# Kernel tuning notes

Measured on AMD Instinct MI355X. Metric: run time of the kernel, lower is better.

## Reference

```python
import jax, jax.numpy as jnp
import numpy as np

B, S, E = 2, 2048, 2048
H, KV, D = 16, 4, 128
G = H // KV  # query heads per kv head
THETA = 10000.0


def setup_inputs() -> dict:
    key = jax.random.key(0)
    ks = jax.random.split(key, 5)
    scale = 0.02
    return {
        "x": jax.random.normal(ks[0], (B, S, E), dtype=jnp.float32),
        "Wq": jax.random.normal(ks[1], (E, H * D), dtype=jnp.float32) * scale,
        "Wk": jax.random.normal(ks[2], (E, KV * D), dtype=jnp.float32) * scale,
        "Wv": jax.random.normal(ks[3], (E, KV * D), dtype=jnp.float32) * scale,
        "Wo": jax.random.normal(ks[4], (E, E), dtype=jnp.float32) * scale,
    }


def _rope_tables(seq_len, head_dim, theta):
    inv_freq = 1.0 / theta ** (jnp.arange(0, head_dim, 2, dtype=jnp.float32) / head_dim)
    t = jnp.arange(seq_len, dtype=jnp.float32)
    freqs = jnp.outer(t, inv_freq)  # [S, D/2]
    cos = jnp.concatenate([jnp.cos(freqs), jnp.cos(freqs)], axis=-1)  # [S, D]
    sin = jnp.concatenate([jnp.sin(freqs), jnp.sin(freqs)], axis=-1)
    return cos, sin


def _apply_rope(x, cos, sin):
    # x: [B, h, S, D]; cos/sin: [S, D] broadcast over batch/heads
    d2 = x.shape[-1] // 2
    x1, x2 = x[..., :d2], x[..., d2:]
    rotated = jnp.concatenate([-x2, x1], axis=-1)
    return x * cos + rotated * sin


def reference(x, Wq, Wk, Wv, Wo):
    b, s, _ = x.shape
    q = (x @ Wq).reshape(b, s, H, D).transpose(0, 2, 1, 3)   # [B,H,S,D]
    k = (x @ Wk).reshape(b, s, KV, D).transpose(0, 2, 1, 3)  # [B,KV,S,D]
    v = (x @ Wv).reshape(b, s, KV, D).transpose(0, 2, 1, 3)

    cos, sin = _rope_tables(s, D, THETA)
    q = _apply_rope(q, cos, sin)
    k = _apply_rope(k, cos, sin)

    # GQA: q head h attends to kv head h // G (repeat_interleave order)
    qg = q.reshape(b, KV, G, s, D)
    scores = jnp.einsum("bkgsd,bktd->bkgst", qg, k) / jnp.sqrt(jnp.asarray(D, x.dtype))
    causal = jnp.tril(jnp.ones((s, s), dtype=bool))
    scores = jnp.where(causal, scores, jnp.asarray(-jnp.inf, scores.dtype))
    attn = jax.nn.softmax(scores, axis=-1)
    out = jnp.einsum("bkgst,bktd->bkgsd", attn, v)  # [B,KV,G,S,D]
    out = out.reshape(b, H, s, D).transpose(0, 2, 1, 3).reshape(b, s, H * D)
    return out @ Wo
```

## Files before the change

kernel.cpp:

```cpp
#include <hip/hip_runtime.h>
#include <stdint.h>

#define B_ 2
#define S_ 2048
#define E_ 2048
#define H_ 16
#define KV_ 4
#define D_ 128
#define G_ (H_ / KV_)
#define M_ (B_ * S_)

typedef unsigned short u16;
typedef unsigned int u32;
typedef __bf16 bf16x8 __attribute__((ext_vector_type(8)));
typedef float f32x4 __attribute__((ext_vector_type(4)));

__device__ __forceinline__ u16 f2bf(float f) {
  __bf16 h = (__bf16)f;
  return *(u16*)&h;
}
__device__ __forceinline__ float bf2f(u16 x) {
  return __uint_as_float(((u32)x) << 16);
}
__device__ __forceinline__ void store_c(u16* p, float v) { *p = f2bf(v); }
__device__ __forceinline__ void store_c(float* p, float v) { *p = v; }

__device__ __forceinline__ void gload_lds16(const u16* g, u16* lds) {
  __builtin_amdgcn_global_load_lds((const __attribute__((address_space(1))) u32*)g,
                                   (__attribute__((address_space(3))) u32*)lds,
                                   16, 0, 0);
}

__global__ __launch_bounds__(256) void convert_fp32_bf16(const float4* __restrict__ x,
                                                         uint2* __restrict__ o, int n4) {
  int i = blockIdx.x * 256 + threadIdx.x;
  if (i >= n4) return;
  float4 v = x[i];
  uint2 r;
  r.x = (u32)f2bf(v.x) | ((u32)f2bf(v.y) << 16);
  r.y = (u32)f2bf(v.z) | ((u32)f2bf(v.w) << 16);
  o[i] = r;
}

__global__ __launch_bounds__(256) void transpose_conv_w(const float* __restrict__ W,
                                                        u16* __restrict__ Wt,
                                                        int Kdim, int Ndim) {
  __shared__ float tile[32][33];
  int n0 = blockIdx.x * 32, k0 = blockIdx.y * 32;
  int tx = threadIdx.x, ty = threadIdx.y;
#pragma unroll
  for (int i = 0; i < 4; i++) {
    int r = ty + i * 8;
    tile[r][tx] = W[(size_t)(k0 + r) * Ndim + n0 + tx];
  }
  __syncthreads();
#pragma unroll
  for (int i = 0; i < 4; i++) {
    int r = ty + i * 8;
    Wt[(size_t)(n0 + r) * Kdim + k0 + tx] = f2bf(tile[tx][r]);
  }
}

__global__ __launch_bounds__(256) void transpose_v(const u16* __restrict__ V,
                                                   u16* __restrict__ Vt) {
  __shared__ u16 tile[32][33];
  int bkv = blockIdx.z;
  int b = bkv / KV_, kv = bkv % KV_;
  int s0 = blockIdx.x * 32, d0 = blockIdx.y * 32;
  int tx = threadIdx.x, ty = threadIdx.y;
#pragma unroll
  for (int i = 0; i < 4; i++) {
    int r = ty + i * 8;
    tile[r][tx] = V[((size_t)((b * S_ + s0 + r) * KV_ + kv)) * D_ + d0 + tx];
  }
  __syncthreads();
#pragma unroll
  for (int i = 0; i < 4; i++) {
    int r = ty + i * 8;
    Vt[((size_t)(b * KV_ + kv) * D_ + d0 + r) * S_ + s0 + tx] = tile[tx][r];
  }
}

__global__ __launch_bounds__(256) void rope_k_repack(const u16* __restrict__ Kin,
                                                     u16* __restrict__ Kp, int total) {
  int idx = blockIdx.x * 256 + threadIdx.x;
  if (idx >= total) return;
  int d = idx & 63;
  int rem = idx >> 6;
  int kv = rem % KV_;
  int row = rem / KV_;
  int b = row >> 11;
  int spos = row & (S_ - 1);
  size_t src = ((size_t)row * KV_ + kv) * D_ + d;
  float x0 = bf2f(Kin[src]);
  float x1 = bf2f(Kin[src + 64]);
  float ang = (float)spos * expf(-0.14391156831212787f * (float)d);
  float sn, cs;
  sincosf(ang, &sn, &cs);
  size_t dst = ((size_t)((b * KV_ + kv) * S_ + spos)) * D_ + d;
  Kp[dst]      = f2bf(x0 * cs - x1 * sn);
  Kp[dst + 64] = f2bf(x1 * cs + x0 * sn);
}

__global__ __launch_bounds__(256) void rope_q_inplace(u16* __restrict__ Qb, int total) {
  int idx = blockIdx.x * 256 + threadIdx.x;
  if (idx >= total) return;
  int d = idx & 63;
  int rem = idx >> 6;
  int h = rem & (H_ - 1);
  int row = rem >> 4;
  int spos = row & (S_ - 1);
  size_t base = ((size_t)row * H_ + h) * D_ + d;
  float x0 = bf2f(Qb[base]);
  float x1 = bf2f(Qb[base + 64]);
  float ang = (float)spos * expf(-0.14391156831212787f * (float)d);
  float sn, cs;
  sincosf(ang, &sn, &cs);
  const float scale = 0.08838834764831845f;
  Qb[base]      = f2bf((x0 * cs - x1 * sn) * scale);
  Qb[base + 64] = f2bf((x1 * cs + x0 * sn) * scale);
}

template <typename CT>
__device__ __forceinline__ void gemm256_body(const u16* __restrict__ A,
                                             const u16* __restrict__ Bt,
                                             CT* __restrict__ C,
                                             int Kdim, int Ndim, int m0, int n0) {
  extern __shared__ __align__(16) u16 smem[];
  const int tid  = threadIdx.x;
  const int lane = tid & 63;
  const int wave = tid >> 6;
  const int wm   = wave >> 2;
  const int wn   = wave & 3;
  const int bh   = wn >> 1;
  const int nb   = (wn & 1) * 64;
  const int quad = lane >> 4, lm = lane & 15;

  int soff[2], sldb[2];
#pragma unroll
  for (int i = 0; i < 2; i++) {
    int cc  = i * 512 + tid;
    int row = cc >> 3;
    int q   = (cc & 7) ^ (row & 7);
    soff[i] = row * Kdim + q * 8;
    sldb[i] = (i * 512 + wave * 64) * 8;
  }
  auto STAGE = [&](const u16* g, u16* l) {
    gload_lds16(g + soff[0], l + sldb[0]);
    gload_lds16(g + soff[1], l + sldb[1]);
  };

  int cs0 = ((0 + quad) ^ (lm & 7)) * 8;
  int cs1 = ((4 + quad) ^ (lm & 7)) * 8;

  const u16* Ag = A  + (size_t)m0 * Kdim;
  const u16* Bg = Bt + (size_t)n0 * Kdim;
  const size_t hstep = (size_t)128 * Kdim;

  f32x4 acc[8][4];
  f32x4 zero = {0.f, 0.f, 0.f, 0.f};
#pragma unroll
  for (int m = 0; m < 8; m++)
#pragma unroll
    for (int n = 0; n < 4; n++) acc[m][n] = zero;

  const int NKT = Kdim >> 6;

  STAGE(Bg,             smem + 32768 + 0 * 8192);
  STAGE(Ag,             smem + 0 * 8192);
  STAGE(Ag + hstep,     smem + 1 * 8192);
  STAGE(Bg + hstep,     smem + 32768 + 1 * 8192);
  STAGE(Bg + 64,        smem + 32768 + 2 * 8192);
  STAGE(Ag + 64,        smem + 2 * 8192);
  STAGE(Ag + hstep + 64, smem + 3 * 8192);
  asm volatile("s_waitcnt vmcnt(6)" ::: "memory");
  __builtin_amdgcn_s_barrier();

  for (int kt = 0; kt < NKT; ++kt) {
    const int cur = kt & 1;
    const u16* regA = smem + (cur * 2 + wm) * 8192;
    const u16* regB = smem + 32768 + (cur * 2 + bh) * 8192;
    bf16x8 af[4][2], bf[4][2];

#pragma unroll
    for (int n = 0; n < 4; n++) {
      bf[n][0] = *(const bf16x8*)(regB + (nb + n * 16 + lm) * 64 + cs0);
      bf[n][1] = *(const bf16x8*)(regB + (nb + n * 16 + lm) * 64 + cs1);
    }
#pragma unroll
    for (int m = 0; m < 4; m++) {
      af[m][0] = *(const bf16x8*)(regA + (m * 16 + lm) * 64 + cs0);
      af[m][1] = *(const bf16x8*)(regA + (m * 16 + lm) * 64 + cs1);
    }
    if (kt + 1 < NKT)
      STAGE(Bg + hstep + (size_t)(kt + 1) * 64,
            smem + 32768 + (((kt + 1) & 1) * 2 + 1) * 8192);
    asm volatile("s_waitcnt lgkmcnt(0)" ::: "memory");
    __builtin_amdgcn_s_barrier();
    __builtin_amdgcn_s_setprio(1);
#pragma unroll
    for (int m = 0; m < 4; m++)
#pragma unroll
      for (int n = 0; n < 2; n++) {
        acc[m][n] = __builtin_amdgcn_mfma_f32_16x16x32_bf16(af[m][0], bf[n][0], acc[m][n], 0, 0, 0);
        acc[m][n] = __builtin_amdgcn_mfma_f32_16x16x32_bf16(af[m][1], bf[n][1], acc[m][n], 0, 0, 0);
      }
    __builtin_amdgcn_s_setprio(0);
    __builtin_amdgcn_s_barrier();

    if (kt + 2 < NKT)
      STAGE(Bg + (size_t)(kt + 2) * 64, smem + 32768 + (cur * 2 + 0) * 8192);
    __builtin_amdgcn_s_barrier();
    __builtin_amdgcn_s_setprio(1);
#pragma unroll
    for (int m = 0; m < 4; m++)
#pragma unroll
      for (int n = 2; n < 4; n++) {
        acc[m][n] = __builtin_amdgcn_mfma_f32_16x16x32_bf16(af[m][0], bf[n][0], acc[m][n], 0, 0, 0);
        acc[m][n] = __builtin_amdgcn_mfma_f32_16x16x32_bf16(af[m][1], bf[n][1], acc[m][n], 0, 0, 0);
      }
    __builtin_amdgcn_s_setprio(0);
    __builtin_amdgcn_s_barrier();

#pragma unroll
    for (int m = 0; m < 4; m++) {
      af[m][0] = *(const bf16x8*)(regA + ((m + 4) * 16 + lm) * 64 + cs0);
      af[m][1] = *(const bf16x8*)(regA + ((m + 4) * 16 + lm) * 64 + cs1);
    }
    asm volatile("s_waitcnt lgkmcnt(0)" ::: "memory");
    __builtin_amdgcn_s_barrier();
    __builtin_amdgcn_s_setprio(1);
#pragma unroll
    for (int m = 0; m < 4; m++)
#pragma unroll
      for (int n = 0; n < 2; n++) {
        acc[m + 4][n] = __builtin_amdgcn_mfma_f32_16x16x32_bf16(af[m][0], bf[n][0], acc[m + 4][n], 0, 0, 0);
        acc[m + 4][n] = __builtin_amdgcn_mfma_f32_16x16x32_bf16(af[m][1], bf[n][1], acc[m + 4][n], 0, 0, 0);
      }
    __builtin_amdgcn_s_setprio(0);
    __builtin_amdgcn_s_barrier();

    if (kt + 2 < NKT) {
      STAGE(Ag + (size_t)(kt + 2) * 64,         smem + (cur * 2 + 0) * 8192);
      STAGE(Ag + hstep + (size_t)(kt + 2) * 64, smem + (cur * 2 + 1) * 8192);
    }
    __builtin_amdgcn_s_setprio(1);
#pragma unroll
    for (int m = 0; m < 4; m++)
#pragma unroll
      for (int n = 2; n < 4; n++) {
        acc[m + 4][n] = __builtin_amdgcn_mfma_f32_16x16x32_bf16(af[m][0], bf[n][0], acc[m + 4][n], 0, 0, 0);
        acc[m + 4][n] = __builtin_amdgcn_mfma_f32_16x16x32_bf16(af[m][1], bf[n][1], acc[m + 4][n], 0, 0, 0);
      }
    __builtin_amdgcn_s_setprio(0);
    asm volatile("s_waitcnt vmcnt(6)" ::: "memory");
    __builtin_amdgcn_s_barrier();
  }

#pragma unroll
  for (int m = 0; m < 8; m++) {
    const int row = m0 + wm * 128 + m * 16 + quad * 4;
#pragma unroll
    for (int n = 0; n < 4; n++) {
      const int col = n0 + wn * 64 + n * 16 + lm;
#pragma unroll
      for (int r = 0; r < 4; r++)
        store_c(C + (size_t)(row + r) * Ndim + col, acc[m][n][r]);
    }
  }
}

__global__ __launch_bounds__(512, 2) void gemm256_qkv(const u16* __restrict__ A,
                                                      const u16* __restrict__ WqT,
                                                      const u16* __restrict__ WkT,
                                                      const u16* __restrict__ WvT,
                                                      u16* __restrict__ Qb,
                                                      u16* __restrict__ Kb,
                                                      u16* __restrict__ Vb) {
  int bx = blockIdx.x;
  const u16* Bt;
  u16* C;
  int n0, Ndim;
  if (bx < 8)       { Bt = WqT; C = Qb; n0 = bx * 256;        Ndim = 2048; }
  else if (bx < 10) { Bt = WkT; C = Kb; n0 = (bx - 8) * 256;  Ndim = 512; }
  else              { Bt = WvT; C = Vb; n0 = (bx - 10) * 256; Ndim = 512; }
  gemm256_body<u16>(A, Bt, C, 2048, Ndim, blockIdx.y * 256, n0);
}

__global__ __launch_bounds__(512, 2) void gemm256_wo(const u16* __restrict__ A,
                                                     const u16* __restrict__ Bt,
                                                     float* __restrict__ C) {
  gemm256_body<float>(A, Bt, C, 2048, 2048, blockIdx.y * 256, blockIdx.x * 256);
}

__global__ __launch_bounds__(256, 2) void attn_kernel(const u16* __restrict__ Q,
                                                      const u16* __restrict__ Kp,
                                                      const u16* __restrict__ Vt,
                                                      u16* __restrict__ O) {
  __shared__ __align__(16) u16 Ksh[2][64 * 128];
  __shared__ __align__(16) u16 Vsh[2][128 * 64];
  __shared__ __align__(16) u16 Psh[4][16 * 64];

  const int tid = threadIdx.x;
  const int lane = tid & 63;
  const int wave = tid >> 6;
  const int quad = lane >> 4, lm = lane & 15;
  const int b = blockIdx.z, h = blockIdx.x;
  const int kh = h / G_;

  const u16* Kbase = Kp + (size_t)(b * KV_ + kh) * S_ * D_;
  const u16* Vbase = Vt + (size_t)(b * KV_ + kh) * D_ * S_;
  u16* pw = &Psh[wave][0];

  int offK[4], offV[4], ldsOff[4];
#pragma unroll
  for (int i = 0; i < 4; i++) {
    int idx = (wave * 4 + i) * 64 + lane;
    int rK = idx >> 4;
    int cK = (idx & 15) ^ (rK & 7);
    offK[i] = rK * 128 + cK * 8;
    int rV = idx >> 3;
    int cV = (idx & 7) ^ (rV & 7);
    offV[i] = rV * S_ + cV * 8;
    ldsOff[i] = (wave * 4 + i) * 512;
  }

  bf16x8 onesb;
#pragma unroll
  for (int j = 0; j < 8; j++) onesb[j] = (__bf16)1.0f;

#pragma unroll
  for (int half = 0; half < 2; half++) {
    const int qi = half ? blockIdx.y : (31 - blockIdx.y);
    const int sq0 = qi * 64;
    const int nT = qi + 1;
    const int wrow = sq0 + wave * 16;

    const u16* qptr = Q + ((size_t)(b * S_ + wrow + lm) * H_ + h) * D_;
    bf16x8 qf[4];
#pragma unroll
    for (int ks = 0; ks < 4; ks++)
      qf[ks] = *(const bf16x8*)(qptr + ks * 32 + quad * 8);

    f32x4 o[8];
    f32x4 lacc = {0.f, 0.f, 0.f, 0.f};
#pragma unroll
    for (int i = 0; i < 8; i++) o[i] = f32x4{0.f, 0.f, 0.f, 0.f};

    __syncthreads();

#pragma unroll
    for (int i = 0; i < 4; i++)
      gload_lds16(Kbase + offK[i], &Ksh[0][ldsOff[i]]);
#pragma unroll
    for (int i = 0; i < 4; i++)
      gload_lds16(Vbase + offV[i], &Vsh[0][ldsOff[i]]);

    for (int t = 0; t < nT; t++) {
      const int sk0 = t << 6;

      __builtin_amdgcn_s_barrier();

      if (t + 1 < nT) {
        const u16* kg = Kbase + (size_t)(t + 1) * 64 * 128;
        const u16* vg = Vbase + (t + 1) * 64;
        u16* kb_next = &Ksh[(t + 1) & 1][0];
        u16* vb_next = &Vsh[(t + 1) & 1][0];
#pragma unroll
        for (int i = 0; i < 4; i++)
          gload_lds16(kg + offK[i], kb_next + ldsOff[i]);
#pragma unroll
        for (int i = 0; i < 4; i++)
          gload_lds16(vg + offV[i], vb_next + ldsOff[i]);
        asm volatile("s_waitcnt vmcnt(8)" ::: "memory");
      } else {
        asm volatile("s_waitcnt vmcnt(0)" ::: "memory");
      }

      __builtin_amdgcn_s_barrier();
      __builtin_amdgcn_sched_barrier(0);

      const u16* kbuf = &Ksh[t & 1][0];
      f32x4 sc[4];
#pragma unroll
      for (int nt = 0; nt < 4; nt++) sc[nt] = f32x4{0.f, 0.f, 0.f, 0.f};
      __builtin_amdgcn_s_setprio(1);
#pragma unroll
      for (int ks = 0; ks < 4; ks++) {
#pragma unroll
        for (int nt = 0; nt < 4; nt++) {
          int R = nt * 16 + lm;
          bf16x8 kb = *(const bf16x8*)(kbuf + R * 128 + (((ks * 4 + quad) ^ (R & 7)) * 8));
          sc[nt] = __builtin_amdgcn_mfma_f32_16x16x32_bf16(qf[ks], kb, sc[nt], 0, 0, 0);
        }
      }
      __builtin_amdgcn_s_setprio(0);
      const bool nm = (sk0 + 63 > wrow);
#pragma unroll
      for (int nt = 0; nt < 4; nt++)
#pragma unroll
        for (int r = 0; r < 4; r++) {
          float p = __expf(sc[nt][r]);
          if (nm) {
            int kc = sk0 + nt * 16 + lm;
            int qr = wrow + quad * 4 + r;
            p = (kc > qr) ? 0.f : p;
          }
          sc[nt][r] = p;
        }
#pragma unroll
      for (int nt = 0; nt < 4; nt++)
#pragma unroll
        for (int r = 0; r < 4; r++) {
          int p = quad * 4 + r;
          int c = nt * 2 + (lm >> 3);
          pw[p * 64 + ((c ^ (p & 7)) * 8) + (lm & 7)] = f2bf(sc[nt][r]);
        }
      const u16* vbuf = &Vsh[t & 1][0];
      __builtin_amdgcn_s_setprio(1);
#pragma unroll
      for (int ks = 0; ks < 2; ks++) {
        int pr = lm;
        bf16x8 pa = *(const bf16x8*)(pw + pr * 64 + (((ks * 4 + quad) ^ (pr & 7)) * 8));
        lacc = __builtin_amdgcn_mfma_f32_16x16x32_bf16(pa, onesb, lacc, 0, 0, 0);
#pragma unroll
        for (int d8 = 0; d8 < 8; d8++) {
          int R = d8 * 16 + lm;
          bf16x8 vb = *(const bf16x8*)(vbuf + R * 64 + (((ks * 4 + quad) ^ (R & 7)) * 8));
          o[d8] = __builtin_amdgcn_mfma_f32_16x16x32_bf16(pa, vb, o[d8], 0, 0, 0);
        }
      }
      __builtin_amdgcn_s_setprio(0);
    }

    float inv[4];
#pragma unroll
    for (int r = 0; r < 4; r++) inv[r] = 1.0f / lacc[r];
#pragma unroll
    for (int d8 = 0; d8 < 8; d8++)
#pragma unroll
      for (int r = 0; r < 4; r++) {
        int srow = wrow + quad * 4 + r;
        O[((size_t)(b * S_ + srow) * H_ + h) * D_ + d8 * 16 + lm] = f2bf(o[d8][r] * inv[r]);
      }
  }
}

extern "C" void kernel_launch(void* const* d_in, const int* in_sizes, int n_in,
                              void* d_out, int out_size, void* d_ws, size_t ws_size,
                              hipStream_t stream) {
  const float* x  = (const float*)d_in[0];
  const float* Wq = (const float*)d_in[1];
  const float* Wk = (const float*)d_in[2];
  const float* Wv = (const float*)d_in[3];
  const float* Wo = (const float*)d_in[4];
  float* out = (float*)d_out;
  char* ws = (char*)d_ws;
  u16* Xb  = (u16*)(ws);
  u16* WqT = (u16*)(ws + (16ull << 20));
  u16* WkT = (u16*)(ws + (24ull << 20));
  u16* WvT = (u16*)(ws + (26ull << 20));
  u16* WoT = (u16*)(ws + (28ull << 20));
  u16* Qb  = (u16*)(ws + (36ull << 20));
  u16* Kb  = (u16*)(ws + (52ull << 20));
  u16* Vb  = (u16*)(ws + (56ull << 20));
  u16* Vt  = (u16*)(ws + (60ull << 20));
  u16* Ob  = (u16*)(ws + (64ull << 20));
  u16* Kp  = (u16*)(ws + (80ull << 20));

  static bool attr_set = false;
  if (!attr_set) {
    hipFuncSetAttribute((const void*)gemm256_qkv,
                        hipFuncAttributeMaxDynamicSharedMemorySize, 131072);
    hipFuncSetAttribute((const void*)gemm256_wo,
                        hipFuncAttributeMaxDynamicSharedMemorySize, 131072);
    attr_set = true;
  }

  dim3 tb32(32, 8);

  convert_fp32_bf16<<<dim3(M_ * E_ / 4 / 256), 256, 0, stream>>>((const float4*)x, (uint2*)Xb, M_ * E_ / 4);
  transpose_conv_w<<<dim3(2048 / 32, 2048 / 32), tb32, 0, stream>>>(Wq, WqT, E_, H_ * D_);
  transpose_conv_w<<<dim3(512 / 32, 2048 / 32), tb32, 0, stream>>>(Wk, WkT, E_, KV_ * D_);
  transpose_conv_w<<<dim3(512 / 32, 2048 / 32), tb32, 0, stream>>>(Wv, WvT, E_, KV_ * D_);
  transpose_conv_w<<<dim3(2048 / 32, 2048 / 32), tb32, 0, stream>>>(Wo, WoT, E_, E_);

  gemm256_qkv<<<dim3(12, M_ / 256), 512, 131072, stream>>>(Xb, WqT, WkT, WvT, Qb, Kb, Vb);

  rope_q_inplace<<<dim3(M_ * H_ * 64 / 256), 256, 0, stream>>>(Qb, M_ * H_ * 64);

  rope_k_repack<<<dim3(M_ * KV_ * 64 / 256), 256, 0, stream>>>(Kb, Kp, M_ * KV_ * 64);

  transpose_v<<<dim3(S_ / 32, D_ / 32, B_ * KV_), tb32, 0, stream>>>(Vb, Vt);

  attn_kernel<<<dim3(H_, 16, B_), 256, 0, stream>>>(Qb, Kp, Vt, Ob);

  gemm256_wo<<<dim3(2048 / 256, M_ / 256), 512, 131072, stream>>>(Ob, WoT, out);
}
```

Before: 318.6 us.

## Software-pipeline attention loop: overlap next tile's QK^T with current softmax/PV

Restructures the causal attention inner loop so the QK^T MFMAs for tile t+1 are issued before the exp/mask/PV work for tile t. Two score register sets alternate between iterations. K and V loads are now split and issued two tiles ahead, with waits adjusted to match. The aim is to hide the latency of the exp and the LDS round-trip for P behind matrix work. The cost is higher register pressure from the extra score set, plus more intricate barrier and vmcnt logic that must stay correct.

New measurement: 321.9 us. No clear change (+1.0%).

```diff
diff --git a/kernel.cpp b/kernel.cpp
--- a/kernel.cpp
+++ b/kernel.cpp
@@ -346,44 +346,12 @@
     f32x4 lacc = {0.f, 0.f, 0.f, 0.f};
 #pragma unroll
     for (int i = 0; i < 8; i++) o[i] = f32x4{0.f, 0.f, 0.f, 0.f};
-
-    __syncthreads();
-
-#pragma unroll
-    for (int i = 0; i < 4; i++)
-      gload_lds16(Kbase + offK[i], &Ksh[0][ldsOff[i]]);
-#pragma unroll
-    for (int i = 0; i < 4; i++)
-      gload_lds16(Vbase + offV[i], &Vsh[0][ldsOff[i]]);
-
-    for (int t = 0; t < nT; t++) {
-      const int sk0 = t << 6;
-
-      __builtin_amdgcn_s_barrier();
-
-      if (t + 1 < nT) {
-        const u16* kg = Kbase + (size_t)(t + 1) * 64 * 128;
-        const u16* vg = Vbase + (t + 1) * 64;
-        u16* kb_next = &Ksh[(t + 1) & 1][0];
-        u16* vb_next = &Vsh[(t + 1) & 1][0];
-#pragma unroll
-        for (int i = 0; i < 4; i++)
-          gload_lds16(kg + offK[i], kb_next + ldsOff[i]);
-#pragma unroll
-        for (int i = 0; i < 4; i++)
-          gload_lds16(vg + offV[i], vb_next + ldsOff[i]);
-        asm volatile("s_waitcnt vmcnt(8)" ::: "memory");
-      } else {
-        asm volatile("s_waitcnt vmcnt(0)" ::: "memory");
-      }
-
-      __builtin_amdgcn_s_barrier();
-      __builtin_amdgcn_sched_barrier(0);
-
-      const u16* kbuf = &Ksh[t & 1][0];
-      f32x4 sc[4];
-#pragma unroll
-      for (int nt = 0; nt < 4; nt++) sc[nt] = f32x4{0.f, 0.f, 0.f, 0.f};
+    f32x4 scA[4], scB[4];
+
+    auto QKT = [&](int tt, f32x4 (&s)[4]) {
+      const u16* kbuf = &Ksh[tt & 1][0];
+#pragma unroll
+      for (int nt = 0; nt < 4; nt++) s[nt] = f32x4{0.f, 0.f, 0.f, 0.f};
       __builtin_amdgcn_s_setprio(1);
 #pragma unroll
       for (int ks = 0; ks < 4; ks++) {
@@ -391,22 +359,26 @@
         for (int nt = 0; nt < 4; nt++) {
           int R = nt * 16 + lm;
           bf16x8 kb = *(const bf16x8*)(kbuf + R * 128 + (((ks * 4 + quad) ^ (R & 7)) * 8));
-          sc[nt] = __builtin_amdgcn_mfma_f32_16x16x32_bf16(qf[ks], kb, sc[nt], 0, 0, 0);
+          s[nt] = __builtin_amdgcn_mfma_f32_16x16x32_bf16(qf[ks], kb, s[nt], 0, 0, 0);
         }
       }
       __builtin_amdgcn_s_setprio(0);
+    };
+
+    auto SMPV = [&](int t, f32x4 (&s)[4]) {
+      const int sk0 = t << 6;
       const bool nm = (sk0 + 63 > wrow);
 #pragma unroll
       for (int nt = 0; nt < 4; nt++)
 #pragma unroll
         for (int r = 0; r < 4; r++) {
-          float p = __expf(sc[nt][r]);
+          float p = __expf(s[nt][r]);
           if (nm) {
             int kc = sk0 + nt * 16 + lm;
             int qr = wrow + quad * 4 + r;
             p = (kc > qr) ? 0.f : p;
           }
-          sc[nt][r] = p;
+          s[nt][r] = p;
         }
 #pragma unroll
       for (int nt = 0; nt < 4; nt++)
@@ -414,7 +386,7 @@
         for (int r = 0; r < 4; r++) {
           int p = quad * 4 + r;
           int c = nt * 2 + (lm >> 3);
-          pw[p * 64 + ((c ^ (p & 7)) * 8) + (lm & 7)] = f2bf(sc[nt][r]);
+          pw[p * 64 + ((c ^ (p & 7)) * 8) + (lm & 7)] = f2bf(s[nt][r]);
         }
       const u16* vbuf = &Vsh[t & 1][0];
       __builtin_amdgcn_s_setprio(1);
@@ -431,6 +403,62 @@
         }
       }
       __builtin_amdgcn_s_setprio(0);
+    };
+
+    auto ITER = [&](int t, f32x4 (&scC)[4], f32x4 (&scN)[4]) {
+      __builtin_amdgcn_s_barrier();
+      if (t + 2 < nT) {
+        const u16* kg = Kbase + (size_t)(t + 2) * 64 * 128;
+        u16* kb2 = &Ksh[t & 1][0];
+#pragma unroll
+        for (int i = 0; i < 4; i++)
+          gload_lds16(kg + offK[i], kb2 + ldsOff[i]);
+      }
+      __builtin_amdgcn_sched_barrier(0);
+      if (t + 1 < nT) QKT(t + 1, scN);
+      SMPV(t, scC);
+      __builtin_amdgcn_s_barrier();
+      if (t + 2 < nT) {
+        const u16* vg = Vbase + (t + 2) * 64;
+        u16* vb2 = &Vsh[t & 1][0];
+#pragma unroll
+        for (int i = 0; i < 4; i++)
+          gload_lds16(vg + offV[i], vb2 + ldsOff[i]);
+        asm volatile("s_waitcnt vmcnt(4)" ::: "memory");
+      } else {
+        asm volatile("s_waitcnt vmcnt(0)" ::: "memory");
+      }
+      __builtin_amdgcn_sched_barrier(0);
+    };
+
+    __syncthreads();
+
+#pragma unroll
+    for (int i = 0; i < 4; i++)
+      gload_lds16(Kbase + offK[i], &Ksh[0][ldsOff[i]]);
+#pragma unroll
+    for (int i = 0; i < 4; i++)
+      gload_lds16(Vbase + offV[i], &Vsh[0][ldsOff[i]]);
+    if (nT > 1) {
+      const u16* kg = Kbase + (size_t)64 * 128;
+#pragma unroll
+      for (int i = 0; i < 4; i++)
+        gload_lds16(kg + offK[i], &Ksh[1][ldsOff[i]]);
+#pragma unroll
+      for (int i = 0; i < 4; i++)
+        gload_lds16(Vbase + 64 + offV[i], &Vsh[1][ldsOff[i]]);
+      asm volatile("s_waitcnt vmcnt(4)" ::: "memory");
+    } else {
+      asm volatile("s_waitcnt vmcnt(0)" ::: "memory");
+    }
+    __builtin_amdgcn_s_barrier();
+    __builtin_amdgcn_sched_barrier(0);
+
+    QKT(0, scA);
+
+    for (int t = 0; t < nT; t += 2) {
+      ITER(t, scA, scB);
+      if (t + 1 < nT) ITER(t + 1, scB, scA);
     }
 
     float inv[4];
```

## Use 256x128 tiles for output projection GEMM to fill all CUs

Applied to the files above, without the earlier changes.

Replaces the 256x256-tile Wo GEMM with a dedicated 256x128-tile kernel. This doubles the block count so the grid covers more of the GPU's compute units instead of leaving half idle. The kernel keeps the double-buffered LDS staging with swizzled layout and interleaved MFMA/load phases, and lowers shared memory to 96KB. Smaller N tiles reduce per-block data reuse and increase total global traffic for A.

New measurement: 297.9 us. 6.5% less time.

```diff
diff --git a/kernel.cpp b/kernel.cpp
--- a/kernel.cpp
+++ b/kernel.cpp
@@ -287,10 +287,161 @@
   gemm256_body<u16>(A, Bt, C, 2048, Ndim, blockIdx.y * 256, n0);
 }
 
-__global__ __launch_bounds__(512, 2) void gemm256_wo(const u16* __restrict__ A,
-                                                     const u16* __restrict__ Bt,
-                                                     float* __restrict__ C) {
-  gemm256_body<float>(A, Bt, C, 2048, 2048, blockIdx.y * 256, blockIdx.x * 256);
+__global__ __launch_bounds__(512, 2) void gemm256x128_wo(const u16* __restrict__ A,
+                                                         const u16* __restrict__ Bt,
+                                                         float* __restrict__ C) {
+  extern __shared__ __align__(16) u16 smem[];
+  const int Kdim = 2048, Ndim = 2048;
+  const int m0 = blockIdx.y * 256, n0 = blockIdx.x * 128;
+  const int tid  = threadIdx.x;
+  const int lane = tid & 63;
+  const int wave = tid >> 6;
+  const int wm   = wave >> 2;
+  const int wn   = wave & 3;
+  const int bh   = wn >> 1;
+  const int nb   = (wn & 1) * 32;
+  const int quad = lane >> 4, lm = lane & 15;
+
+  int soffA[2], sldbA[2];
+#pragma unroll
+  for (int i = 0; i < 2; i++) {
+    int cc  = i * 512 + tid;
+    int row = cc >> 3;
+    int q   = (cc & 7) ^ (row & 7);
+    soffA[i] = row * Kdim + q * 8;
+    sldbA[i] = (i * 512 + wave * 64) * 8;
+  }
+  const int rowB = tid >> 3;
+  const int soffB = rowB * Kdim + (((tid & 7) ^ (rowB & 7)) * 8);
+  const int sldbB = wave * 512;
+  auto STAGE_A = [&](const u16* g, u16* l) {
+    gload_lds16(g + soffA[0], l + sldbA[0]);
+    gload_lds16(g + soffA[1], l + sldbA[1]);
+  };
+  auto STAGE_B = [&](const u16* g, u16* l) {
+    gload_lds16(g + soffB, l + sldbB);
+  };
+
+  int cs0 = ((0 + quad) ^ (lm & 7)) * 8;
+  int cs1 = ((4 + quad) ^ (lm & 7)) * 8;
+
+  const u16* Ag = A  + (size_t)m0 * Kdim;
+  const u16* Bg = Bt + (size_t)n0 * Kdim;
+  const size_t hstepA = (size_t)128 * Kdim;
+  const size_t hstepB = (size_t)64 * Kdim;
+
+  f32x4 acc[8][2];
+  f32x4 zero = {0.f, 0.f, 0.f, 0.f};
+#pragma unroll
+  for (int m = 0; m < 8; m++) {
+    acc[m][0] = zero;
+    acc[m][1] = zero;
+  }
+
+  const int NKT = Kdim >> 6;
+
+  STAGE_B(Bg,              smem + 32768 + 0 * 4096);
+  STAGE_A(Ag,              smem + 0 * 8192);
+  STAGE_A(Ag + hstepA,     smem + 1 * 8192);
+  STAGE_B(Bg + hstepB,     smem + 32768 + 1 * 4096);
+  STAGE_B(Bg + 64,         smem + 32768 + 2 * 4096);
+  STAGE_A(Ag + 64,         smem + 2 * 8192);
+  STAGE_A(Ag + hstepA + 64, smem + 3 * 8192);
+  asm volatile("s_waitcnt vmcnt(5)" ::: "memory");
+  __builtin_amdgcn_s_barrier();
+
+  for (int kt = 0; kt < NKT; ++kt) {
+    const int cur = kt & 1;
+    const u16* regA = smem + (cur * 2 + wm) * 8192;
+    const u16* regB = smem + 32768 + (cur * 2 + bh) * 4096;
+    bf16x8 af[4][2], bf[2][2];
+
+#pragma unroll
+    for (int n = 0; n < 2; n++) {
+      bf[n][0] = *(const bf16x8*)(regB + (nb + n * 16 + lm) * 64 + cs0);
+      bf[n][1] = *(const bf16x8*)(regB + (nb + n * 16 + lm) * 64 + cs1);
+    }
+#pragma unroll
+    for (int m = 0; m < 4; m++) {
+      af[m][0] = *(const bf16x8*)(regA + (m * 16 + lm) * 64 + cs0);
+      af[m][1] = *(const bf16x8*)(regA + (m * 16 + lm) * 64 + cs1);
+    }
+    if (kt + 1 < NKT)
+      STAGE_B(Bg + hstepB + (size_t)(kt + 1) * 64,
+              smem + 32768 + (((kt + 1) & 1) * 2 + 1) * 4096);
+    asm volatile("s_waitcnt lgkmcnt(0)" ::: "memory");
+    __builtin_amdgcn_s_barrier();
+    __builtin_amdgcn_s_setprio(1);
+#pragma unroll
+    for (int m = 0; m < 2; m++)
+#pragma unroll
+      for (int n = 0; n < 2; n++) {
+        acc[m][n] = __builtin_amdgcn_mfma_f32_16x16x32_bf16(af[m][0], bf[n][0], acc[m][n], 0, 0, 0);
+        acc[m][n] = __builtin_amdgcn_mfma_f32_16x16x32_bf16(af[m][1], bf[n][1], acc[m][n], 0, 0, 0);
+      }
+    __builtin_amdgcn_s_setprio(0);
+    __builtin_amdgcn_s_barrier();
+
+    if (kt + 2 < NKT)
+      STAGE_B(Bg + (size_t)(kt + 2) * 64, smem + 32768 + (cur * 2 + 0) * 4096);
+    __builtin_amdgcn_s_barrier();
+    __builtin_amdgcn_s_setprio(1);
+#pragma unroll
+    for (int m = 2; m < 4; m++)
+#pragma unroll
+      for (int n = 0; n < 2; n++) {
+        acc[m][n] = __builtin_amdgcn_mfma_f32_16x16x32_bf16(af[m][0], bf[n][0], acc[m][n], 0, 0, 0);
+        acc[m][n] = __builtin_amdgcn_mfma_f32_16x16x32_bf16(af[m][1], bf[n][1], acc[m][n], 0, 0, 0);
+      }
+    __builtin_amdgcn_s_setprio(0);
+    __builtin_amdgcn_s_barrier();
+
+#pragma unroll
+    for (int m = 0; m < 4; m++) {
+      af[m][0] = *(const bf16x8*)(regA + ((m + 4) * 16 + lm) * 64 + cs0);
+      af[m][1] = *(const bf16x8*)(regA + ((m + 4) * 16 + lm) * 64 + cs1);
+    }
+    asm volatile("s_waitcnt lgkmcnt(0)" ::: "memory");
+    __builtin_amdgcn_s_barrier();
+    __builtin_amdgcn_s_setprio(1);
+#pragma unroll
+    for (int m = 0; m < 2; m++)
+#pragma unroll
+      for (int n = 0; n < 2; n++) {
+        acc[m + 4][n] = __builtin_amdgcn_mfma_f32_16x16x32_bf16(af[m][0], bf[n][0], acc[m + 4][n], 0, 0, 0);
+        acc[m + 4][n] = __builtin_amdgcn_mfma_f32_16x16x32_bf16(af[m][1], bf[n][1], acc[m + 4][n], 0, 0, 0);
+      }
+    __builtin_amdgcn_s_setprio(0);
+    __builtin_amdgcn_s_barrier();
+
+    if (kt + 2 < NKT) {
+      STAGE_A(Ag + (size_t)(kt + 2) * 64,          smem + (cur * 2 + 0) * 8192);
+      STAGE_A(Ag + hstepA + (size_t)(kt + 2) * 64, smem + (cur * 2 + 1) * 8192);
+    }
+    __builtin_amdgcn_s_setprio(1);
+#pragma unroll
+    for (int m = 2; m < 4; m++)
+#pragma unroll
+      for (int n = 0; n < 2; n++) {
+        acc[m + 4][n] = __builtin_amdgcn_mfma_f32_16x16x32_bf16(af[m][0], bf[n][0], acc[m + 4][n], 0, 0, 0);
+        acc[m + 4][n] = __builtin_amdgcn_mfma_f32_16x16x32_bf16(af[m][1], bf[n][1], acc[m + 4][n], 0, 0, 0);
+      }
+    __builtin_amdgcn_s_setprio(0);
+    asm volatile("s_waitcnt vmcnt(5)" ::: "memory");
+    __builtin_amdgcn_s_barrier();
+  }
+
+#pragma unroll
+  for (int m = 0; m < 8; m++) {
+    const int row = m0 + wm * 128 + m * 16 + quad * 4;
+#pragma unroll
+    for (int n = 0; n < 2; n++) {
+      const int col = n0 + wn * 32 + n * 16 + lm;
+#pragma unroll
+      for (int r = 0; r < 4; r++)
+        C[(size_t)(row + r) * Ndim + col] = acc[m][n][r];
+    }
+  }
 }
 
 __global__ __launch_bounds__(256, 2) void attn_kernel(const u16* __restrict__ Q,
@@ -472,8 +623,8 @@
   if (!attr_set) {
     hipFuncSetAttribute((const void*)gemm256_qkv,
                         hipFuncAttributeMaxDynamicSharedMemorySize, 131072);
-    hipFuncSetAttribute((const void*)gemm256_wo,
-                        hipFuncAttributeMaxDynamicSharedMemorySize, 131072);
+    hipFuncSetAttribute((const void*)gemm256x128_wo,
+                        hipFuncAttributeMaxDynamicSharedMemorySize, 98304);
     attr_set = true;
   }
 
@@ -495,5 +646,5 @@
 
   attn_kernel<<<dim3(H_, 16, B_), 256, 0, stream>>>(Qb, Kp, Vt, Ob);
 
-  gemm256_wo<<<dim3(2048 / 256, M_ / 256), 512, 131072, stream>>>(Ob, WoT, out);
-}
+  gemm256x128_wo<<<dim3(2048 / 128, M_ / 256), 512, 98304, stream>>>(Ob, WoT, out);
+}
```
